# Optimization experiments

Hardware: AMD Instinct MI355X
Metric: run time of the kernel (lower is better)

The kernel has to match this reference:

```python
import jax, jax.numpy as jnp
import numpy as np

KS = 3      # kernel_size
PAD = 1     # padding
DIL = 2     # dilation


def conv2d(x, w, b=None, stride=1, padding=0):
    out = jax.lax.conv_general_dilated(
        x, w, (stride, stride), [(padding, padding)] * 2,
        dimension_numbers=("NCHW", "OIHW", "NCHW"))
    if b is not None:
        out = out + b[None, :, None, None]
    return out


def setup_inputs() -> dict:
    key = jax.random.key(0)
    ks = jax.random.split(key, 6)
    b, inc, outc, H, W = 2, 256, 256, 96, 96
    x = jax.random.normal(ks[0], (b, inc, H, W), jnp.float32)
    w_p = jax.random.normal(ks[1], (2 * KS * KS, inc, 3, 3), jnp.float32) * 0.01
    b_p = jax.random.normal(ks[2], (2 * KS * KS,), jnp.float32) * 0.01
    w_ad = jax.random.normal(ks[3], (KS, inc, 3, 3), jnp.float32) * 0.01
    b_ad = jax.random.normal(ks[4], (KS,), jnp.float32) * 0.01
    w_conv = jax.random.normal(ks[5], (outc, inc, KS, KS), jnp.float32) * 0.02
    return {"x": x, "w_p": w_p, "b_p": b_p, "w_ad": w_ad, "b_ad": b_ad, "w_conv": w_conv}


def reference(x, w_p, b_p, w_ad, b_ad, w_conv):
    b, c, H, W = x.shape
    N = KS * KS

    offset = conv2d(x, w_p, b_p, stride=1, padding=1)                    # [b,2N,H,W]
    ad_base = 1.0 - jax.nn.sigmoid(conv2d(x, w_ad, b_ad, stride=1, padding=1))  # [b,KS,H,W]
    ad = jnp.tile(ad_base, (1, 2 * KS, 1, 1)) * DIL                      # [b,2N,H,W]

    # p_n: per-kernel-tap offsets (x-part first, then y-part), meshgrid 'ij'
    r = jnp.arange(-(KS - 1) // 2, (KS - 1) // 2 + 1, dtype=jnp.float32)
    pnx, pny = jnp.meshgrid(r, r, indexing="ij")
    p_n = jnp.concatenate([pnx.ravel(), pny.ravel()])[None, :, None, None]  # [1,2N,1,1]

    # p_0: base sampling grid in padded-image coords (starts at 1)
    p0x = jnp.broadcast_to(jnp.arange(1, H + 1, dtype=jnp.float32)[:, None], (H, W))
    p0y = jnp.broadcast_to(jnp.arange(1, W + 1, dtype=jnp.float32)[None, :], (H, W))
    p_0 = jnp.concatenate([jnp.tile(p0x[None, None], (1, N, 1, 1)),
                           jnp.tile(p0y[None, None], (1, N, 1, 1))], axis=1)  # [1,2N,H,W]

    p = p_0 + p_n + offset + ad * p_n                                    # [b,2N,H,W]
    p = jnp.transpose(p, (0, 2, 3, 1))                                   # [b,H,W,2N]

    xp = jnp.pad(x, ((0, 0), (0, 0), (PAD, PAD), (PAD, PAD)))
    Hp, Wp = xp.shape[2], xp.shape[3]

    q_lt = jnp.floor(jax.lax.stop_gradient(p))
    q_rb = q_lt + 1

    def clampxy(q):
        return jnp.concatenate([jnp.clip(q[..., :N], 0, Hp - 1),
                                jnp.clip(q[..., N:], 0, Wp - 1)], -1).astype(jnp.int32)

    q_lt = clampxy(q_lt)
    q_rb = clampxy(q_rb)
    q_lb = jnp.concatenate([q_lt[..., :N], q_rb[..., N:]], -1)
    q_rt = jnp.concatenate([q_rb[..., :N], q_lt[..., N:]], -1)

    mask = jnp.concatenate(
        [(p[..., :N] < PAD) | (p[..., :N] > Hp - 1 - PAD),
         (p[..., N:] < PAD) | (p[..., N:] > Wp - 1 - PAD)], -1)
    mask = jax.lax.stop_gradient(mask).astype(p.dtype)
    floor_p = p - (p - jnp.floor(p))  # == floor(p) but with zero gradient, as in torch
    p = p * (1 - mask) + floor_p * mask
    p = jnp.concatenate([jnp.clip(p[..., :N], 0, Hp - 1),
                         jnp.clip(p[..., N:], 0, Wp - 1)], -1)

    px, py = p[..., :N], p[..., N:]
    f = lambda q: q.astype(p.dtype)
    g_lt = (1 + (f(q_lt[..., :N]) - px)) * (1 + (f(q_lt[..., N:]) - py))
    g_rb = (1 - (f(q_rb[..., :N]) - px)) * (1 - (f(q_rb[..., N:]) - py))
    g_lb = (1 + (f(q_lb[..., :N]) - px)) * (1 - (f(q_lb[..., N:]) - py))
    g_rt = (1 - (f(q_rt[..., :N]) - px)) * (1 + (f(q_rt[..., N:]) - py))

    xf = xp.reshape(b, c, Hp * Wp)

    def gather(xb, q):  # xb [c,L], q [H,W,2N] -> [c,H,W,N]
        idx = q[..., :N] * Wp + q[..., N:]
        return xb[:, idx]

    gq = jax.vmap(gather)
    x_lt = gq(xf, q_lt)
    x_rb = gq(xf, q_rb)
    x_lb = gq(xf, q_lb)
    x_rt = gq(xf, q_rt)

    x_off = (g_lt[:, None] * x_lt + g_rb[:, None] * x_rb +
             g_lb[:, None] * x_lb + g_rt[:, None] * x_rt)  # [b,c,H,W,N]

    # N index k = kx*KS + ky -> place at (i*KS+kx, j*KS+ky)
    x_off = x_off.reshape(b, c, H, W, KS, KS)
    x_off = jnp.transpose(x_off, (0, 1, 2, 4, 3, 5)).reshape(b, c, H * KS, W * KS)

    return conv2d(x_off, w_conv, None, stride=KS, padding=0)  # [b,outc,H,W]
```

## Files before the change

kernel.cpp:

```cpp
#include <hip/hip_runtime.h>
#include <math.h>

typedef unsigned short u16;
typedef unsigned int   u32;

typedef __attribute__((ext_vector_type(8))) _Float16 f16x8;
typedef __attribute__((ext_vector_type(4))) float    f32x4;

#define NB   2
#define C    256
#define H    96
#define W    96
#define HW   (H*W)
#define HP   98
#define OC   256
#define KDIM (9*C)
#define NS   (NB*HW)

#define XP_OFF    0
#define AHI_OFF   19668992
#define ALO_OFF   20848640
#define A2HI_OFF  22028288
#define A2LO_OFF  22175744
#define OFF2_OFF  22323200
#define IDX_OFF   23871488
#define G_OFF     26525696

__device__ __forceinline__ u16 h2u(_Float16 h) {
  return __builtin_bit_cast(unsigned short, h);
}
__device__ __forceinline__ void split16(float v, u16& hi, u16& lo) {
  _Float16 h = (_Float16)v;
  float r = v - (float)h;
  _Float16 l = (_Float16)r;
  hi = h2u(h); lo = h2u(l);
}
__device__ __forceinline__ void sync_lds() {
  asm volatile("s_waitcnt lgkmcnt(0)\n\ts_barrier" ::: "memory");
}

__global__ __launch_bounds__(256) void prep1(
    const float* __restrict__ x, const float* __restrict__ w_p,
    const float* __restrict__ w_ad, const float* __restrict__ w_conv,
    float* __restrict__ xp,
    u16* __restrict__ A_hi, u16* __restrict__ A_lo,
    u16* __restrict__ A2_hi, u16* __restrict__ A2_lo) {
  __shared__ float smem[64*65];
  int bx = blockIdx.x;
  int tid = threadIdx.x;

  if (bx < 1152) {
    int pb = bx;
    int n = pb / 576; int r = pb % 576;
    int cb = r / 144; int hwb = r % 144;
    int c0 = cb * 64, hw0 = hwb * 64;
    int ii = tid & 63; int cl4 = tid >> 6;
    #pragma unroll
    for (int r2 = 0; r2 < 16; r2++) {
      int c_l = cl4*16 + r2;
      smem[c_l*65 + ii] = x[(size_t)(n*C + c0 + c_l)*HW + hw0 + ii];
    }
    __syncthreads();
    int hw = hw0 + ii;
    int h = hw / W, w = hw % W;
    float* dst = xp + ((size_t)(n*HP + h + 1)*HP + (w + 1))*C + c0 + cl4*16;
    #pragma unroll
    for (int q = 0; q < 4; q++) {
      *(float4*)(dst + q*4) = make_float4(smem[(cl4*16 + q*4 + 0)*65 + ii],
                                          smem[(cl4*16 + q*4 + 1)*65 + ii],
                                          smem[(cl4*16 + q*4 + 2)*65 + ii],
                                          smem[(cl4*16 + q*4 + 3)*65 + ii]);
    }

  } else if (bx < 1440) {
    int pb = bx - 1152;
    int t = pb*256 + tid;
    int e0 = t*8;
    int lane = (e0 >> 3) & 63;
    int mi   = (e0 >> 9) & 3;
    int mw   = (e0 >> 11) & 1;
    int rr   = e0 >> 12; int itg = rr % 72; int mo = rr / 72;
    int o = mo*128 + mw*64 + mi*16 + (lane & 15);
    int kcb = itg*32 + (lane >> 4)*8;
    #pragma unroll
    for (int j2 = 0; j2 < 8; j2++) {
      int kc = kcb + j2; int k = kc >> 8; int c = kc & 255;
      float a = w_conv[((size_t)o*C + c)*9 + k];
      u16 hi, lo; split16(a, hi, lo);
      A_hi[e0 + j2] = hi; A_lo[e0 + j2] = lo;
    }

  } else {
    int pb = bx - 1440;
    int t = pb*256 + tid;
    int e0 = t*8;
    int lane = (e0 >> 3) & 63;
    int mi   = (e0 >> 9) & 1;
    int itg  = e0 >> 10;
    int o = mi*16 + (lane & 15);
    int kcb = itg*32 + (lane >> 4)*8;
    #pragma unroll
    for (int j2 = 0; j2 < 8; j2++) {
      int kc = kcb + j2; int tap = kc >> 8; int c = kc & 255;
      float a = 0.f;
      if (o < 18)       a = w_p [((size_t)o*C + c)*9 + tap];
      else if (o < 21)  a = w_ad[((size_t)(o-18)*C + c)*9 + tap];
      u16 hi, lo; split16(a, hi, lo);
      A2_hi[e0 + j2] = hi; A2_lo[e0 + j2] = lo;
    }
  }
}

__global__ __launch_bounds__(256) void conv_mfma(
    const u16* __restrict__ A2_hi, const u16* __restrict__ A2_lo,
    const float* __restrict__ xp, float* __restrict__ off2) {
  int bx = blockIdx.x;
  int xcd = bx & 7; int jj = bx >> 3;
  int kh = jj & 3; int sbl = jj >> 2;
  int sb = xcd*36 + sbl;
  int s0 = sb * 64;
  int tid = threadIdx.x;
  int wave = tid >> 6, lane = tid & 63;
  int l16 = lane & 15, quad = lane >> 4;

  f32x4 acc[2];
  f32x4 z4 = {0.f, 0.f, 0.f, 0.f};
  acc[0] = z4; acc[1] = z4;

  int sg = s0 + wave*16 + l16;
  int n = sg / HW; int hw = sg % HW;
  int h = hw / W, w = hw % W;
  const float* sbase = xp + ((size_t)(n*HP + h)*HP + w)*C + quad*8;

  for (int it = 0; it < 18; it++) {
    int itg = kh*18 + it;
    int tap = itg >> 3;
    int di = tap / 3, dj = tap % 3;
    int c0k = (itg & 7) * 32;
    uint4 aH[2], aL[2];
    #pragma unroll
    for (int mi = 0; mi < 2; mi++) {
      size_t off = ((size_t)(itg*2 + mi) << 9) + lane*8;
      aH[mi] = *(const uint4*)(A2_hi + off);
      aL[mi] = *(const uint4*)(A2_lo + off);
    }
    const float* p0 = sbase + (di*HP + dj)*C + c0k;
    float4 ta = *(const float4*)(p0), tb = *(const float4*)(p0 + 4);
    float v[8] = {ta.x, ta.y, ta.z, ta.w, tb.x, tb.y, tb.z, tb.w};
    u16 hb[8], lb[8];
    #pragma unroll
    for (int j = 0; j < 8; j++) split16(v[j], hb[j], lb[j]);
    uint4 bph, bpl;
    bph.x = (u32)hb[0] | ((u32)hb[1] << 16); bph.y = (u32)hb[2] | ((u32)hb[3] << 16);
    bph.z = (u32)hb[4] | ((u32)hb[5] << 16); bph.w = (u32)hb[6] | ((u32)hb[7] << 16);
    bpl.x = (u32)lb[0] | ((u32)lb[1] << 16); bpl.y = (u32)lb[2] | ((u32)lb[3] << 16);
    bpl.z = (u32)lb[4] | ((u32)lb[5] << 16); bpl.w = (u32)lb[6] | ((u32)lb[7] << 16);
    f16x8 bfh = __builtin_bit_cast(f16x8, bph);
    f16x8 bfl = __builtin_bit_cast(f16x8, bpl);
    #pragma unroll
    for (int mi = 0; mi < 2; mi++) {
      f16x8 fh = __builtin_bit_cast(f16x8, aH[mi]);
      f16x8 fl = __builtin_bit_cast(f16x8, aL[mi]);
      acc[mi] = __builtin_amdgcn_mfma_f32_16x16x32_f16(fh, bfh, acc[mi], 0, 0, 0);
      acc[mi] = __builtin_amdgcn_mfma_f32_16x16x32_f16(fh, bfl, acc[mi], 0, 0, 0);
      acc[mi] = __builtin_amdgcn_mfma_f32_16x16x32_f16(fl, bfh, acc[mi], 0, 0, 0);
    }
  }
  int sout = s0 + wave*16 + l16;
  #pragma unroll
  for (int mi = 0; mi < 2; mi++)
    #pragma unroll
    for (int rr2 = 0; rr2 < 4; rr2++) {
      int o = mi*16 + quad*4 + rr2;
      if (o < 21)
        atomicAdd(&off2[(size_t)o*NS + sout], acc[mi][rr2]);
    }
}

__global__ __launch_bounds__(256) void taps2(
    const float* __restrict__ off2, const float* __restrict__ b_p,
    const float* __restrict__ b_ad,
    int* __restrict__ idx_arr, float* __restrict__ g_arr) {
  int e = blockIdx.x * 256 + threadIdx.x;
  int k = e / NS; int s = e % NS;
  int n = s / HW; int hw = s % HW;
  int h = hw / W, w = hw % W;
  float offx = off2[(size_t)k*NS + s]            + b_p[k];
  float offy = off2[(size_t)(k+9)*NS + s]        + b_p[k+9];
  float za   = off2[(size_t)(18 + (k%3))*NS + s] + b_ad[k % 3];
  float a2 = 2.0f / (1.0f + expf(za));

  float ri = (float)(k / 3) - 1.0f, rj = (float)(k % 3) - 1.0f;
  float px = (float)(h + 1) + ri + offx + a2 * ri;
  float py = (float)(w + 1) + rj + offy + a2 * rj;
  float fx = floorf(px), fy = floorf(py);
  int qltx = min(max((int)fx, 0), 97);
  int qlty = min(max((int)fy, 0), 97);
  int qrbx = min(max((int)fx + 1, 0), 97);
  int qrby = min(max((int)fy + 1, 0), 97);
  bool mx = (px < 1.0f) || (px > 96.0f);
  bool my = (py < 1.0f) || (py > 96.0f);
  float pxm = mx ? fx : px;
  float pym = my ? fy : py;
  pxm = fminf(fmaxf(pxm, 0.f), 97.f);
  pym = fminf(fmaxf(pym, 0.f), 97.f);
  float glx = 1.0f + ((float)qltx - pxm);
  float grx = 1.0f - ((float)qrbx - pxm);
  float gly = 1.0f + ((float)qlty - pym);
  float gry = 1.0f - ((float)qrby - pym);
  int base = n * HP * HP * C;
  int4 qi;
  qi.x = base + (qltx*HP + qlty)*C;
  qi.y = base + (qrbx*HP + qrby)*C;
  qi.z = base + (qltx*HP + qrby)*C;
  qi.w = base + (qrbx*HP + qlty)*C;
  float4 gg = make_float4(glx*gly, grx*gry, glx*gry, grx*gly);
  *(int4*)(idx_arr + (size_t)e*4) = qi;
  *(float4*)(g_arr  + (size_t)e*4) = gg;
}

__global__ __launch_bounds__(256) void gemm_def(
    const u16* __restrict__ A_hi,
    const float* __restrict__ xp,
    const int* __restrict__ idx_arr, const float* __restrict__ g_arr,
    float* __restrict__ out) {
  __shared__ u16 Bh[2][64*40];
  int bx = blockIdx.x;
  int xcd = bx & 7; int jj = bx >> 3;
  int kh = jj & 1; int sbl = jj >> 1;
  int sb = xcd*36 + sbl;
  int s0 = sb * 64;
  int n = s0 / HW; int hw0 = s0 % HW;
  int tid = threadIdx.x;
  int wave = tid >> 6, lane = tid & 63;
  int l16 = lane & 15, quad = lane >> 4;
  int mo = wave >> 1, mw = wave & 1;

  f32x4 acc[4][4];
  f32x4 z4 = {0.f, 0.f, 0.f, 0.f};
  #pragma unroll
  for (int i = 0; i < 4; i++)
    { acc[i][0] = z4; acc[i][1] = z4; acc[i][2] = z4; acc[i][3] = z4; }

  int s_l = tid >> 2; int cs = (tid & 3) * 8;
  int sg = s0 + s_l;

  int4 qi; float4 gg;
  for (int it = 0; it < 36; it++) {
    int itg = kh*36 + it;
    int c0k = (itg & 7) * 32;
    if (it == 0 || (itg & 7) == 0) {
      int k = itg >> 3;
      qi = *(const int4*)(idx_arr + ((size_t)k*NS + sg)*4);
      gg = *(const float4*)(g_arr  + ((size_t)k*NS + sg)*4);
    }
    uint4 aH[4];
    int abase = ((mo*72 + itg)*2 + mw)*4;
    #pragma unroll
    for (int mi = 0; mi < 4; mi++) {
      size_t off = ((size_t)(abase + mi) << 9) + lane*8;
      aH[mi] = *(const uint4*)(A_hi + off);
    }
    const float* p0 = xp + qi.x + c0k + cs;
    const float* p1 = xp + qi.y + c0k + cs;
    const float* p2 = xp + qi.z + c0k + cs;
    const float* p3 = xp + qi.w + c0k + cs;
    float4 t0a = *(const float4*)(p0), t0b = *(const float4*)(p0 + 4);
    float4 t1a = *(const float4*)(p1), t1b = *(const float4*)(p1 + 4);
    float4 t2a = *(const float4*)(p2), t2b = *(const float4*)(p2 + 4);
    float4 t3a = *(const float4*)(p3), t3b = *(const float4*)(p3 + 4);
    float v[8];
    v[0] = gg.x*t0a.x + gg.y*t1a.x + gg.z*t2a.x + gg.w*t3a.x;
    v[1] = gg.x*t0a.y + gg.y*t1a.y + gg.z*t2a.y + gg.w*t3a.y;
    v[2] = gg.x*t0a.z + gg.y*t1a.z + gg.z*t2a.z + gg.w*t3a.z;
    v[3] = gg.x*t0a.w + gg.y*t1a.w + gg.z*t2a.w + gg.w*t3a.w;
    v[4] = gg.x*t0b.x + gg.y*t1b.x + gg.z*t2b.x + gg.w*t3b.x;
    v[5] = gg.x*t0b.y + gg.y*t1b.y + gg.z*t2b.y + gg.w*t3b.y;
    v[6] = gg.x*t0b.z + gg.y*t1b.z + gg.z*t2b.z + gg.w*t3b.z;
    v[7] = gg.x*t0b.w + gg.y*t1b.w + gg.z*t2b.w + gg.w*t3b.w;
    u16 hb[8];
    #pragma unroll
    for (int j = 0; j < 8; j++) hb[j] = h2u((_Float16)v[j]);
    uint4 bph;
    bph.x = (u32)hb[0] | ((u32)hb[1] << 16); bph.y = (u32)hb[2] | ((u32)hb[3] << 16);
    bph.z = (u32)hb[4] | ((u32)hb[5] << 16); bph.w = (u32)hb[6] | ((u32)hb[7] << 16);
    int buf = it & 1;
    *(uint4*)(&Bh[buf][s_l*40 + cs]) = bph;
    sync_lds();
    f16x8 bfh[4];
    #pragma unroll
    for (int ni = 0; ni < 4; ni++) {
      int rr = (ni*16 + l16)*40 + quad*8;
      bfh[ni] = *(const f16x8*)(&Bh[buf][rr]);
    }
    #pragma unroll
    for (int mi = 0; mi < 4; mi++) {
      f16x8 fh = __builtin_bit_cast(f16x8, aH[mi]);
      #pragma unroll
      for (int ni = 0; ni < 4; ni++) {
        acc[mi][ni] = __builtin_amdgcn_mfma_f32_16x16x32_f16(fh, bfh[ni], acc[mi][ni], 0, 0, 0);
      }
    }
  }
  #pragma unroll
  for (int mi = 0; mi < 4; mi++)
    #pragma unroll
    for (int ni = 0; ni < 4; ni++) {
      int hw = hw0 + ni*16 + l16;
      #pragma unroll
      for (int rr = 0; rr < 4; rr++) {
        int o = wave*64 + mi*16 + quad*4 + rr;
        atomicAdd(&out[(size_t)(n*OC + o)*HW + hw], acc[mi][ni][rr]);
      }
    }
}

extern "C" void kernel_launch(void* const* d_in, const int* in_sizes, int n_in,
                              void* d_out, int out_size, void* d_ws, size_t ws_size,
                              hipStream_t stream) {
  const float* x      = (const float*)d_in[0];
  const float* w_p    = (const float*)d_in[1];
  const float* b_p    = (const float*)d_in[2];
  const float* w_ad   = (const float*)d_in[3];
  const float* b_ad   = (const float*)d_in[4];
  const float* w_conv = (const float*)d_in[5];
  float* out = (float*)d_out;

  char* ws = (char*)d_ws;
  float* xp      = (float*)(ws + XP_OFF);
  u16*   A_hi    = (u16*)  (ws + AHI_OFF);
  u16*   A_lo    = (u16*)  (ws + ALO_OFF);
  u16*   A2_hi   = (u16*)  (ws + A2HI_OFF);
  u16*   A2_lo   = (u16*)  (ws + A2LO_OFF);
  float* off2    = (float*)(ws + OFF2_OFF);
  int*   idx_arr = (int*)  (ws + IDX_OFF);
  float* g_arr   = (float*)(ws + G_OFF);

  hipMemsetAsync(xp, 0, (size_t)NB*HP*HP*C*sizeof(float), stream);
  hipMemsetAsync(off2, 0, (size_t)21*NS*sizeof(float), stream);
  hipMemsetAsync(out, 0, (size_t)out_size*sizeof(float), stream);

  prep1    <<<1476, 256, 0, stream>>>(x, w_p, w_ad, w_conv, xp, A_hi, A_lo, A2_hi, A2_lo);
  conv_mfma<<<1152, 256, 0, stream>>>(A2_hi, A2_lo, xp, off2);
  taps2    <<<648,  256, 0, stream>>>(off2, b_p, b_ad, idx_arr, g_arr);
  gemm_def <<<576,  256, 0, stream>>>(A_hi, xp, idx_arr, g_arr, out);
}
```

Measured before the change: 209.1 us.

## Fuse tap computation into deformable GEMM and process two K-slices per sync

Removes the separate taps2 kernel and computes the bilinear indices and weights inside gemm_def straight from the offset-conv output, so the idx/g arrays are never written to or read back from global memory. The main loop also now covers two 32-channel K slices per iteration, with four LDS buffers, which halves the number of barriers and issues more loads before each sync. The cost is that each K-row group redoes the tap math per block, and register use grows from holding twice the A fragments and gathered values, which may lower occupancy.

```diff
diff --git a/kernel.cpp b/kernel.cpp
--- a/kernel.cpp
+++ b/kernel.cpp
@@ -177,19 +177,14 @@
     }
 }
 
-__global__ __launch_bounds__(256) void taps2(
+__device__ __forceinline__ void calc_taps(
     const float* __restrict__ off2, const float* __restrict__ b_p,
     const float* __restrict__ b_ad,
-    int* __restrict__ idx_arr, float* __restrict__ g_arr) {
-  int e = blockIdx.x * 256 + threadIdx.x;
-  int k = e / NS; int s = e % NS;
-  int n = s / HW; int hw = s % HW;
-  int h = hw / W, w = hw % W;
-  float offx = off2[(size_t)k*NS + s]            + b_p[k];
-  float offy = off2[(size_t)(k+9)*NS + s]        + b_p[k+9];
-  float za   = off2[(size_t)(18 + (k%3))*NS + s] + b_ad[k % 3];
+    int k, int sg, int n, int h, int w, int4& qi, float4& gg) {
+  float offx = off2[(size_t)k*NS + sg]            + b_p[k];
+  float offy = off2[(size_t)(k+9)*NS + sg]        + b_p[k+9];
+  float za   = off2[(size_t)(18 + (k%3))*NS + sg] + b_ad[k % 3];
   float a2 = 2.0f / (1.0f + expf(za));
-
   float ri = (float)(k / 3) - 1.0f, rj = (float)(k % 3) - 1.0f;
   float px = (float)(h + 1) + ri + offx + a2 * ri;
   float py = (float)(w + 1) + rj + offy + a2 * rj;
@@ -209,28 +204,43 @@
   float gly = 1.0f + ((float)qlty - pym);
   float gry = 1.0f - ((float)qrby - pym);
   int base = n * HP * HP * C;
-  int4 qi;
   qi.x = base + (qltx*HP + qlty)*C;
   qi.y = base + (qrbx*HP + qrby)*C;
   qi.z = base + (qltx*HP + qrby)*C;
   qi.w = base + (qrbx*HP + qlty)*C;
-  float4 gg = make_float4(glx*gly, grx*gry, glx*gry, grx*gly);
-  *(int4*)(idx_arr + (size_t)e*4) = qi;
-  *(float4*)(g_arr  + (size_t)e*4) = gg;
-}
+  gg = make_float4(glx*gly, grx*gry, glx*gry, grx*gly);
+}
+
+#define BW_SLICE(T0A,T0B,T1A,T1B,T2A,T2B,T3A,T3B, G, BUFI) do { \
+  float v0_ = (G).x*(T0A).x + (G).y*(T1A).x + (G).z*(T2A).x + (G).w*(T3A).x; \
+  float v1_ = (G).x*(T0A).y + (G).y*(T1A).y + (G).z*(T2A).y + (G).w*(T3A).y; \
+  float v2_ = (G).x*(T0A).z + (G).y*(T1A).z + (G).z*(T2A).z + (G).w*(T3A).z; \
+  float v3_ = (G).x*(T0A).w + (G).y*(T1A).w + (G).z*(T2A).w + (G).w*(T3A).w; \
+  float v4_ = (G).x*(T0B).x + (G).y*(T1B).x + (G).z*(T2B).x + (G).w*(T3B).x; \
+  float v5_ = (G).x*(T0B).y + (G).y*(T1B).y + (G).z*(T2B).y + (G).w*(T3B).y; \
+  float v6_ = (G).x*(T0B).z + (G).y*(T1B).z + (G).z*(T2B).z + (G).w*(T3B).z; \
+  float v7_ = (G).x*(T0B).w + (G).y*(T1B).w + (G).z*(T2B).w + (G).w*(T3B).w; \
+  uint4 bph_; \
+  bph_.x = (u32)h2u((_Float16)v0_) | ((u32)h2u((_Float16)v1_) << 16); \
+  bph_.y = (u32)h2u((_Float16)v2_) | ((u32)h2u((_Float16)v3_) << 16); \
+  bph_.z = (u32)h2u((_Float16)v4_) | ((u32)h2u((_Float16)v5_) << 16); \
+  bph_.w = (u32)h2u((_Float16)v6_) | ((u32)h2u((_Float16)v7_) << 16); \
+  *(uint4*)(&Bh[BUFI][s_l*40 + cs]) = bph_; \
+} while (0)
 
 __global__ __launch_bounds__(256) void gemm_def(
     const u16* __restrict__ A_hi,
     const float* __restrict__ xp,
-    const int* __restrict__ idx_arr, const float* __restrict__ g_arr,
+    const float* __restrict__ off2,
+    const float* __restrict__ b_p, const float* __restrict__ b_ad,
     float* __restrict__ out) {
-  __shared__ u16 Bh[2][64*40];
+  __shared__ u16 Bh[4][64*40];
   int bx = blockIdx.x;
   int xcd = bx & 7; int jj = bx >> 3;
   int kh = jj & 1; int sbl = jj >> 1;
   int sb = xcd*36 + sbl;
   int s0 = sb * 64;
-  int n = s0 / HW; int hw0 = s0 % HW;
+  int n0 = s0 / HW; int hw0 = s0 % HW;
   int tid = threadIdx.x;
   int wave = tid >> 6, lane = tid & 63;
   int l16 = lane & 15, quad = lane >> 4;
@@ -244,61 +254,55 @@
 
   int s_l = tid >> 2; int cs = (tid & 3) * 8;
   int sg = s0 + s_l;
+  int n_s = sg / HW; int hw_s = sg % HW;
+  int h_s = hw_s / W, w_s = hw_s % W;
 
   int4 qi; float4 gg;
-  for (int it = 0; it < 36; it++) {
-    int itg = kh*36 + it;
+  for (int t = 0; t < 18; t++) {
+    int itg = kh*36 + 2*t;
     int c0k = (itg & 7) * 32;
-    if (it == 0 || (itg & 7) == 0) {
-      int k = itg >> 3;
-      qi = *(const int4*)(idx_arr + ((size_t)k*NS + sg)*4);
-      gg = *(const float4*)(g_arr  + ((size_t)k*NS + sg)*4);
-    }
-    uint4 aH[4];
-    int abase = ((mo*72 + itg)*2 + mw)*4;
+    if (t == 0 || (itg & 7) == 0) {
+      calc_taps(off2, b_p, b_ad, itg >> 3, sg, n_s, h_s, w_s, qi, gg);
+    }
+    uint4 aH0[4], aH1[4];
+    int abase0 = ((mo*72 + itg)*2 + mw)*4;
+    int abase1 = ((mo*72 + itg + 1)*2 + mw)*4;
     #pragma unroll
     for (int mi = 0; mi < 4; mi++) {
-      size_t off = ((size_t)(abase + mi) << 9) + lane*8;
-      aH[mi] = *(const uint4*)(A_hi + off);
+      aH0[mi] = *(const uint4*)(A_hi + (((size_t)(abase0 + mi)) << 9) + lane*8);
+      aH1[mi] = *(const uint4*)(A_hi + (((size_t)(abase1 + mi)) << 9) + lane*8);
     }
     const float* p0 = xp + qi.x + c0k + cs;
     const float* p1 = xp + qi.y + c0k + cs;
     const float* p2 = xp + qi.z + c0k + cs;
     const float* p3 = xp + qi.w + c0k + cs;
-    float4 t0a = *(const float4*)(p0), t0b = *(const float4*)(p0 + 4);
-    float4 t1a = *(const float4*)(p1), t1b = *(const float4*)(p1 + 4);
-    float4 t2a = *(const float4*)(p2), t2b = *(const float4*)(p2 + 4);
-    float4 t3a = *(const float4*)(p3), t3b = *(const float4*)(p3 + 4);
-    float v[8];
-    v[0] = gg.x*t0a.x + gg.y*t1a.x + gg.z*t2a.x + gg.w*t3a.x;
-    v[1] = gg.x*t0a.y + gg.y*t1a.y + gg.z*t2a.y + gg.w*t3a.y;
-    v[2] = gg.x*t0a.z + gg.y*t1a.z + gg.z*t2a.z + gg.w*t3a.z;
-    v[3] = gg.x*t0a.w + gg.y*t1a.w + gg.z*t2a.w + gg.w*t3a.w;
-    v[4] = gg.x*t0b.x + gg.y*t1b.x + gg.z*t2b.x + gg.w*t3b.x;
-    v[5] = gg.x*t0b.y + gg.y*t1b.y + gg.z*t2b.y + gg.w*t3b.y;
-    v[6] = gg.x*t0b.z + gg.y*t1b.z + gg.z*t2b.z + gg.w*t3b.z;
-    v[7] = gg.x*t0b.w + gg.y*t1b.w + gg.z*t2b.w + gg.w*t3b.w;
-    u16 hb[8];
-    #pragma unroll
-    for (int j = 0; j < 8; j++) hb[j] = h2u((_Float16)v[j]);
-    uint4 bph;
-    bph.x = (u32)hb[0] | ((u32)hb[1] << 16); bph.y = (u32)hb[2] | ((u32)hb[3] << 16);
-    bph.z = (u32)hb[4] | ((u32)hb[5] << 16); bph.w = (u32)hb[6] | ((u32)hb[7] << 16);
-    int buf = it & 1;
-    *(uint4*)(&Bh[buf][s_l*40 + cs]) = bph;
+    float4 t0a0 = *(const float4*)(p0),      t0b0 = *(const float4*)(p0 + 4);
+    float4 t1a0 = *(const float4*)(p1),      t1b0 = *(const float4*)(p1 + 4);
+    float4 t2a0 = *(const float4*)(p2),      t2b0 = *(const float4*)(p2 + 4);
+    float4 t3a0 = *(const float4*)(p3),      t3b0 = *(const float4*)(p3 + 4);
+    float4 t0a1 = *(const float4*)(p0 + 32), t0b1 = *(const float4*)(p0 + 36);
+    float4 t1a1 = *(const float4*)(p1 + 32), t1b1 = *(const float4*)(p1 + 36);
+    float4 t2a1 = *(const float4*)(p2 + 32), t2b1 = *(const float4*)(p2 + 36);
+    float4 t3a1 = *(const float4*)(p3 + 32), t3b1 = *(const float4*)(p3 + 36);
+    int bufb = (t & 1) * 2;
+    BW_SLICE(t0a0,t0b0,t1a0,t1b0,t2a0,t2b0,t3a0,t3b0, gg, bufb);
+    BW_SLICE(t0a1,t0b1,t1a1,t1b1,t2a1,t2b1,t3a1,t3b1, gg, bufb + 1);
     sync_lds();
-    f16x8 bfh[4];
+    f16x8 bfh0[4], bfh1[4];
     #pragma unroll
     for (int ni = 0; ni < 4; ni++) {
       int rr = (ni*16 + l16)*40 + quad*8;
-      bfh[ni] = *(const f16x8*)(&Bh[buf][rr]);
+      bfh0[ni] = *(const f16x8*)(&Bh[bufb][rr]);
+      bfh1[ni] = *(const f16x8*)(&Bh[bufb + 1][rr]);
     }
     #pragma unroll
     for (int mi = 0; mi < 4; mi++) {
-      f16x8 fh = __builtin_bit_cast(f16x8, aH[mi]);
+      f16x8 fh0 = __builtin_bit_cast(f16x8, aH0[mi]);
+      f16x8 fh1 = __builtin_bit_cast(f16x8, aH1[mi]);
       #pragma unroll
       for (int ni = 0; ni < 4; ni++) {
-        acc[mi][ni] = __builtin_amdgcn_mfma_f32_16x16x32_f16(fh, bfh[ni], acc[mi][ni], 0, 0, 0);
+        acc[mi][ni] = __builtin_amdgcn_mfma_f32_16x16x32_f16(fh0, bfh0[ni], acc[mi][ni], 0, 0, 0);
+        acc[mi][ni] = __builtin_amdgcn_mfma_f32_16x16x32_f16(fh1, bfh1[ni], acc[mi][ni], 0, 0, 0);
       }
     }
   }
@@ -310,7 +314,7 @@
       #pragma unroll
       for (int rr = 0; rr < 4; rr++) {
         int o = wave*64 + mi*16 + quad*4 + rr;
-        atomicAdd(&out[(size_t)(n*OC + o)*HW + hw], acc[mi][ni][rr]);
+        atomicAdd(&out[(size_t)(n0*OC + o)*HW + hw], acc[mi][ni][rr]);
       }
     }
 }
@@ -333,8 +337,6 @@
   u16*   A2_hi   = (u16*)  (ws + A2HI_OFF);
   u16*   A2_lo   = (u16*)  (ws + A2LO_OFF);
   float* off2    = (float*)(ws + OFF2_OFF);
-  int*   idx_arr = (int*)  (ws + IDX_OFF);
-  float* g_arr   = (float*)(ws + G_OFF);
 
   hipMemsetAsync(xp, 0, (size_t)NB*HP*HP*C*sizeof(float), stream);
   hipMemsetAsync(off2, 0, (size_t)21*NS*sizeof(float), stream);
@@ -342,6 +344,5 @@
 
   prep1    <<<1476, 256, 0, stream>>>(x, w_p, w_ad, w_conv, xp, A_hi, A_lo, A2_hi, A2_lo);
   conv_mfma<<<1152, 256, 0, stream>>>(A2_hi, A2_lo, xp, off2);
-  taps2    <<<648,  256, 0, stream>>>(off2, b_p, b_ad, idx_arr, g_arr);
-  gemm_def <<<576,  256, 0, stream>>>(A_hi, xp, idx_arr, g_arr, out);
-}
+  gemm_def <<<576,  256, 0, stream>>>(A_hi, xp, off2, b_p, b_ad, out);
+}
```

Measured after the change: 215.6 us. +3.1%, slower.

## Store padded input pre-split as fp16 hi/lo planes and halve offset-conv K split

Applied to the files above, without the earlier changes.

The padded NHWC input is now written once in prep1 as separate fp16 hi and lo planes instead of fp32. The offset conv loads both planes directly and skips the per-iteration split. The deformable GEMM gathers only the fp16 hi plane, which halves gather bandwidth. The offset conv also moves from a 4-way to a 2-way K split, with fewer blocks and fewer atomics. In exchange the bilinear sampling now reads fp16-rounded inputs, which lowers accuracy of the main GEMM operand slightly.

```diff
diff --git a/kernel.cpp b/kernel.cpp
--- a/kernel.cpp
+++ b/kernel.cpp
@@ -17,7 +17,8 @@
 #define KDIM (9*C)
 #define NS   (NB*HW)
 
-#define XP_OFF    0
+#define XPH_OFF   0
+#define XPL_OFF   9834496
 #define AHI_OFF   19668992
 #define ALO_OFF   20848640
 #define A2HI_OFF  22028288
@@ -42,7 +43,7 @@
 __global__ __launch_bounds__(256) void prep1(
     const float* __restrict__ x, const float* __restrict__ w_p,
     const float* __restrict__ w_ad, const float* __restrict__ w_conv,
-    float* __restrict__ xp,
+    u16* __restrict__ xph, u16* __restrict__ xpl,
     u16* __restrict__ A_hi, u16* __restrict__ A_lo,
     u16* __restrict__ A2_hi, u16* __restrict__ A2_lo) {
   __shared__ float smem[64*65];
@@ -63,14 +64,24 @@
     __syncthreads();
     int hw = hw0 + ii;
     int h = hw / W, w = hw % W;
-    float* dst = xp + ((size_t)(n*HP + h + 1)*HP + (w + 1))*C + c0 + cl4*16;
-    #pragma unroll
-    for (int q = 0; q < 4; q++) {
-      *(float4*)(dst + q*4) = make_float4(smem[(cl4*16 + q*4 + 0)*65 + ii],
-                                          smem[(cl4*16 + q*4 + 1)*65 + ii],
-                                          smem[(cl4*16 + q*4 + 2)*65 + ii],
-                                          smem[(cl4*16 + q*4 + 3)*65 + ii]);
-    }
+    size_t base = ((size_t)(n*HP + h + 1)*HP + (w + 1))*C + c0 + cl4*16;
+    u16 th[16], tl[16];
+    #pragma unroll
+    for (int r2 = 0; r2 < 16; r2++)
+      split16(smem[(cl4*16 + r2)*65 + ii], th[r2], tl[r2]);
+    uint4 ph0, ph1, pl0, pl1;
+    ph0.x = (u32)th[0]  | ((u32)th[1]  << 16); ph0.y = (u32)th[2]  | ((u32)th[3]  << 16);
+    ph0.z = (u32)th[4]  | ((u32)th[5]  << 16); ph0.w = (u32)th[6]  | ((u32)th[7]  << 16);
+    ph1.x = (u32)th[8]  | ((u32)th[9]  << 16); ph1.y = (u32)th[10] | ((u32)th[11] << 16);
+    ph1.z = (u32)th[12] | ((u32)th[13] << 16); ph1.w = (u32)th[14] | ((u32)th[15] << 16);
+    pl0.x = (u32)tl[0]  | ((u32)tl[1]  << 16); pl0.y = (u32)tl[2]  | ((u32)tl[3]  << 16);
+    pl0.z = (u32)tl[4]  | ((u32)tl[5]  << 16); pl0.w = (u32)tl[6]  | ((u32)tl[7]  << 16);
+    pl1.x = (u32)tl[8]  | ((u32)tl[9]  << 16); pl1.y = (u32)tl[10] | ((u32)tl[11] << 16);
+    pl1.z = (u32)tl[12] | ((u32)tl[13] << 16); pl1.w = (u32)tl[14] | ((u32)tl[15] << 16);
+    *(uint4*)(xph + base)     = ph0;
+    *(uint4*)(xph + base + 8) = ph1;
+    *(uint4*)(xpl + base)     = pl0;
+    *(uint4*)(xpl + base + 8) = pl1;
 
   } else if (bx < 1440) {
     int pb = bx - 1152;
@@ -113,10 +124,11 @@
 
 __global__ __launch_bounds__(256) void conv_mfma(
     const u16* __restrict__ A2_hi, const u16* __restrict__ A2_lo,
-    const float* __restrict__ xp, float* __restrict__ off2) {
+    const u16* __restrict__ xph, const u16* __restrict__ xpl,
+    float* __restrict__ off2) {
   int bx = blockIdx.x;
   int xcd = bx & 7; int jj = bx >> 3;
-  int kh = jj & 3; int sbl = jj >> 2;
+  int kh = jj & 1; int sbl = jj >> 1;
   int sb = xcd*36 + sbl;
   int s0 = sb * 64;
   int tid = threadIdx.x;
@@ -130,10 +142,12 @@
   int sg = s0 + wave*16 + l16;
   int n = sg / HW; int hw = sg % HW;
   int h = hw / W, w = hw % W;
-  const float* sbase = xp + ((size_t)(n*HP + h)*HP + w)*C + quad*8;
-
-  for (int it = 0; it < 18; it++) {
-    int itg = kh*18 + it;
+  size_t sboff = ((size_t)(n*HP + h)*HP + w)*C + quad*8;
+  const u16* sbH = xph + sboff;
+  const u16* sbL = xpl + sboff;
+
+  for (int it = 0; it < 36; it++) {
+    int itg = kh*36 + it;
     int tap = itg >> 3;
     int di = tap / 3, dj = tap % 3;
     int c0k = (itg & 7) * 32;
@@ -144,19 +158,9 @@
       aH[mi] = *(const uint4*)(A2_hi + off);
       aL[mi] = *(const uint4*)(A2_lo + off);
     }
-    const float* p0 = sbase + (di*HP + dj)*C + c0k;
-    float4 ta = *(const float4*)(p0), tb = *(const float4*)(p0 + 4);
-    float v[8] = {ta.x, ta.y, ta.z, ta.w, tb.x, tb.y, tb.z, tb.w};
-    u16 hb[8], lb[8];
-    #pragma unroll
-    for (int j = 0; j < 8; j++) split16(v[j], hb[j], lb[j]);
-    uint4 bph, bpl;
-    bph.x = (u32)hb[0] | ((u32)hb[1] << 16); bph.y = (u32)hb[2] | ((u32)hb[3] << 16);
-    bph.z = (u32)hb[4] | ((u32)hb[5] << 16); bph.w = (u32)hb[6] | ((u32)hb[7] << 16);
-    bpl.x = (u32)lb[0] | ((u32)lb[1] << 16); bpl.y = (u32)lb[2] | ((u32)lb[3] << 16);
-    bpl.z = (u32)lb[4] | ((u32)lb[5] << 16); bpl.w = (u32)lb[6] | ((u32)lb[7] << 16);
-    f16x8 bfh = __builtin_bit_cast(f16x8, bph);
-    f16x8 bfl = __builtin_bit_cast(f16x8, bpl);
+    int toff = (di*HP + dj)*C + c0k;
+    f16x8 bfh = *(const f16x8*)(sbH + toff);
+    f16x8 bfl = *(const f16x8*)(sbL + toff);
     #pragma unroll
     for (int mi = 0; mi < 2; mi++) {
       f16x8 fh = __builtin_bit_cast(f16x8, aH[mi]);
@@ -221,7 +225,7 @@
 
 __global__ __launch_bounds__(256) void gemm_def(
     const u16* __restrict__ A_hi,
-    const float* __restrict__ xp,
+    const u16* __restrict__ xph,
     const int* __restrict__ idx_arr, const float* __restrict__ g_arr,
     float* __restrict__ out) {
   __shared__ u16 Bh[2][64*40];
@@ -261,26 +265,16 @@
       size_t off = ((size_t)(abase + mi) << 9) + lane*8;
       aH[mi] = *(const uint4*)(A_hi + off);
     }
-    const float* p0 = xp + qi.x + c0k + cs;
-    const float* p1 = xp + qi.y + c0k + cs;
-    const float* p2 = xp + qi.z + c0k + cs;
-    const float* p3 = xp + qi.w + c0k + cs;
-    float4 t0a = *(const float4*)(p0), t0b = *(const float4*)(p0 + 4);
-    float4 t1a = *(const float4*)(p1), t1b = *(const float4*)(p1 + 4);
-    float4 t2a = *(const float4*)(p2), t2b = *(const float4*)(p2 + 4);
-    float4 t3a = *(const float4*)(p3), t3b = *(const float4*)(p3 + 4);
-    float v[8];
-    v[0] = gg.x*t0a.x + gg.y*t1a.x + gg.z*t2a.x + gg.w*t3a.x;
-    v[1] = gg.x*t0a.y + gg.y*t1a.y + gg.z*t2a.y + gg.w*t3a.y;
-    v[2] = gg.x*t0a.z + gg.y*t1a.z + gg.z*t2a.z + gg.w*t3a.z;
-    v[3] = gg.x*t0a.w + gg.y*t1a.w + gg.z*t2a.w + gg.w*t3a.w;
-    v[4] = gg.x*t0b.x + gg.y*t1b.x + gg.z*t2b.x + gg.w*t3b.x;
-    v[5] = gg.x*t0b.y + gg.y*t1b.y + gg.z*t2b.y + gg.w*t3b.y;
-    v[6] = gg.x*t0b.z + gg.y*t1b.z + gg.z*t2b.z + gg.w*t3b.z;
-    v[7] = gg.x*t0b.w + gg.y*t1b.w + gg.z*t2b.w + gg.w*t3b.w;
+    f16x8 t0 = *(const f16x8*)(xph + qi.x + c0k + cs);
+    f16x8 t1 = *(const f16x8*)(xph + qi.y + c0k + cs);
+    f16x8 t2 = *(const f16x8*)(xph + qi.z + c0k + cs);
+    f16x8 t3 = *(const f16x8*)(xph + qi.w + c0k + cs);
     u16 hb[8];
     #pragma unroll
-    for (int j = 0; j < 8; j++) hb[j] = h2u((_Float16)v[j]);
+    for (int j = 0; j < 8; j++) {
+      float v = gg.x*(float)t0[j] + gg.y*(float)t1[j] + gg.z*(float)t2[j] + gg.w*(float)t3[j];
+      hb[j] = h2u((_Float16)v);
+    }
     uint4 bph;
     bph.x = (u32)hb[0] | ((u32)hb[1] << 16); bph.y = (u32)hb[2] | ((u32)hb[3] << 16);
     bph.z = (u32)hb[4] | ((u32)hb[5] << 16); bph.w = (u32)hb[6] | ((u32)hb[7] << 16);
@@ -327,7 +321,8 @@
   float* out = (float*)d_out;
 
   char* ws = (char*)d_ws;
-  float* xp      = (float*)(ws + XP_OFF);
+  u16*   xph     = (u16*)  (ws + XPH_OFF);
+  u16*   xpl     = (u16*)  (ws + XPL_OFF);
   u16*   A_hi    = (u16*)  (ws + AHI_OFF);
   u16*   A_lo    = (u16*)  (ws + ALO_OFF);
   u16*   A2_hi   = (u16*)  (ws + A2HI_OFF);
@@ -336,12 +331,13 @@
   int*   idx_arr = (int*)  (ws + IDX_OFF);
   float* g_arr   = (float*)(ws + G_OFF);
 
-  hipMemsetAsync(xp, 0, (size_t)NB*HP*HP*C*sizeof(float), stream);
+  hipMemsetAsync(xph, 0, (size_t)NB*HP*HP*C*sizeof(u16), stream);
+  hipMemsetAsync(xpl, 0, (size_t)NB*HP*HP*C*sizeof(u16), stream);
   hipMemsetAsync(off2, 0, (size_t)21*NS*sizeof(float), stream);
   hipMemsetAsync(out, 0, (size_t)out_size*sizeof(float), stream);
 
-  prep1    <<<1476, 256, 0, stream>>>(x, w_p, w_ad, w_conv, xp, A_hi, A_lo, A2_hi, A2_lo);
-  conv_mfma<<<1152, 256, 0, stream>>>(A2_hi, A2_lo, xp, off2);
+  prep1    <<<1476, 256, 0, stream>>>(x, w_p, w_ad, w_conv, xph, xpl, A_hi, A_lo, A2_hi, A2_lo);
+  conv_mfma<<<576,  256, 0, stream>>>(A2_hi, A2_lo, xph, xpl, off2);
   taps2    <<<648,  256, 0, stream>>>(off2, b_p, b_ad, idx_arr, g_arr);
-  gemm_def <<<576,  256, 0, stream>>>(A_hi, xp, idx_arr, g_arr, out);
-}
+  gemm_def <<<576,  256, 0, stream>>>(A_hi, xph, idx_arr, g_arr, out);
+}
```

After: 204.3 us. 1.02x faster.
